# Performance work log

Measured on AMD Instinct MI355X. Metric: run time of the kernel, lower is better.

Reference implementation:

```python
import jax, jax.numpy as jnp
import numpy as np

E = 1_600_000   # edges
D = 64          # edge feature dim
H = 128         # mlp hidden
N = 100_000     # nodes


def setup_inputs() -> dict:
    key = jax.random.key(0)
    k1, k2, k3, k4 = jax.random.split(key, 4)
    edge_index = jax.random.randint(k1, (2, E), 0, N, dtype=jnp.int64)
    edge_attr = jax.random.normal(k2, (E, D), dtype=jnp.float32)
    W1 = jax.random.normal(k3, (D, H), dtype=jnp.float32) / np.sqrt(D).astype(np.float32)
    b1 = jnp.zeros((H,), jnp.float32)
    W2 = jax.random.normal(k4, (H, D), dtype=jnp.float32) / np.sqrt(H).astype(np.float32)
    b2 = jnp.zeros((D,), jnp.float32)
    return {"edge_index": edge_index, "edge_attr": edge_attr, "num_nodes": N,
            "W1": W1, "b1": b1, "W2": W2, "b2": b2}


def reference(edge_index, edge_attr, num_nodes, W1, b1, W2, b2):
    # past_nodes, future_nodes = edge_index
    past, future = edge_index[0], edge_index[1]
    # vstack((edge_attr, edge_attr)) scattered by cat((future, past)) with reduce='sum'
    src = jnp.concatenate([edge_attr, edge_attr], axis=0)          # [2E, D]
    idx = jnp.concatenate([future, past], axis=0)                  # [2E]
    flow_total = jax.ops.segment_sum(src, idx, num_segments=num_nodes)  # [N, D]
    # node_mlp: Linear(D,H) -> ReLU -> Linear(H,D)
    h = jax.nn.relu(flow_total @ W1 + b1)
    return h @ W2 + b2
```

## Files before the change

kernel.cpp:

```cpp
#include <hip/hip_runtime.h>
#include <cstdint>
#include <cstddef>

#define D_FEAT 64
#define H_HID 128

#define NBK_SHIFT 9
#define NBK_MASK 511
#define MAXBKT 256
#define TILE 8192
#define CAP 18432


__global__ __launch_bounds__(1024) void bktcount_kernel(
    const int* __restrict__ idx, int* __restrict__ bktCnt, int twoE) {
  __shared__ int cnt[MAXBKT];
  if (threadIdx.x < MAXBKT) cnt[threadIdx.x] = 0;
  __syncthreads();
  int base = blockIdx.x * TILE;
#pragma unroll
  for (int k = 0; k < TILE / 1024; ++k) {
    int t = base + k * 1024 + threadIdx.x;
    if (t < twoE) atomicAdd(&cnt[idx[t] >> NBK_SHIFT], 1);
  }
  __syncthreads();
  if (threadIdx.x < MAXBKT) {
    int c = cnt[threadIdx.x];
    if (c) atomicAdd(&bktCnt[threadIdx.x], c);
  }
}

__global__ __launch_bounds__(256) void bktscan_kernel(
    const int* __restrict__ bktCnt, int* __restrict__ bktOff,
    int* __restrict__ bktCur, int nbkt) {
  __shared__ int s[256];
  int v = (threadIdx.x < nbkt) ? bktCnt[threadIdx.x] : 0;
  s[threadIdx.x] = v;
  __syncthreads();
  for (int d = 1; d < 256; d <<= 1) {
    int t = (threadIdx.x >= d) ? s[threadIdx.x - d] : 0;
    __syncthreads();
    s[threadIdx.x] += t;
    __syncthreads();
  }
  if (threadIdx.x < nbkt) {
    int e = s[threadIdx.x] - v;
    bktOff[threadIdx.x] = e;
    bktCur[threadIdx.x] = e;
  }
}

__global__ __launch_bounds__(1024) void bktscatter_kernel(
    const int* __restrict__ idx, int* __restrict__ bktCur,
    unsigned int* __restrict__ gbkt, int E, int twoE) {
  __shared__ int cnt[MAXBKT];
  __shared__ int lofs[MAXBKT];
  __shared__ int delta[MAXBKT];
  __shared__ unsigned int sval[TILE];
  __shared__ unsigned short sbid[TILE];

  if (threadIdx.x < MAXBKT) cnt[threadIdx.x] = 0;
  __syncthreads();

  int base = blockIdx.x * TILE;
  int myb[8], myr[8];
  unsigned int myv[8];
  int m = 0;
#pragma unroll
  for (int k = 0; k < 8; ++k) {
    int t = base + k * 1024 + threadIdx.x;
    if (t < twoE) {
      int node = idx[t];
      int b = node >> NBK_SHIFT;
      int e = (t < E) ? t : t - E;
      myb[m] = b;
      myv[m] = ((unsigned int)(node & NBK_MASK) << 21) | (unsigned int)e;
      myr[m] = atomicAdd(&cnt[b], 1);
      ++m;
    }
  }
  __syncthreads();

  {
    int v = (threadIdx.x < MAXBKT) ? cnt[threadIdx.x] : 0;
    if (threadIdx.x < MAXBKT) lofs[threadIdx.x] = v;
    __syncthreads();
    for (int d = 1; d < MAXBKT; d <<= 1) {
      int t = (threadIdx.x >= d && threadIdx.x < MAXBKT) ? lofs[threadIdx.x - d] : 0;
      __syncthreads();
      if (threadIdx.x < MAXBKT) lofs[threadIdx.x] += t;
      __syncthreads();
    }
    if (threadIdx.x < MAXBKT) lofs[threadIdx.x] -= v;
  }
  __syncthreads();

  if (threadIdx.x < MAXBKT) {
    int c = cnt[threadIdx.x];
    int rb = c ? atomicAdd(&bktCur[threadIdx.x], c) : 0;
    delta[threadIdx.x] = rb - lofs[threadIdx.x];
  }
  __syncthreads();

  for (int k = 0; k < m; ++k) {
    int slot = lofs[myb[k]] + myr[k];
    sval[slot] = myv[k];
    sbid[slot] = (unsigned short)myb[k];
  }
  __syncthreads();

  int tot = min(TILE, twoE - base);
  for (int s = threadIdx.x; s < tot; s += 1024) {
    gbkt[delta[sbid[s]] + s] = sval[s];
  }
}

__global__ __launch_bounds__(1024) void bktsort_kernel(
    const int* __restrict__ bktCnt, const int* __restrict__ bktOff,
    unsigned int* __restrict__ gbkt,
    int* __restrict__ deg, int* __restrict__ off_end, int N) {
  __shared__ int hist[512];
  __shared__ int cur[512];
  __shared__ unsigned int sorted[CAP];

  int b = blockIdx.x;
  int base = bktOff[b];
  int sz = bktCnt[b];
  if (sz > CAP) sz = CAP;

  if (threadIdx.x < 512) hist[threadIdx.x] = 0;
  __syncthreads();

  for (int s = threadIdx.x; s < sz; s += 1024)
    atomicAdd(&hist[gbkt[base + s] >> 21], 1);
  __syncthreads();

  {
    int v = (threadIdx.x < 512) ? hist[threadIdx.x] : 0;
    if (threadIdx.x < 512) cur[threadIdx.x] = v;
    __syncthreads();
    for (int d = 1; d < 512; d <<= 1) {
      int t = (threadIdx.x >= d && threadIdx.x < 512) ? cur[threadIdx.x - d] : 0;
      __syncthreads();
      if (threadIdx.x < 512) cur[threadIdx.x] += t;
      __syncthreads();
    }
    if (threadIdx.x < 512) cur[threadIdx.x] -= v;
  }
  __syncthreads();

  for (int s = threadIdx.x; s < sz; s += 1024) {
    unsigned int v = gbkt[base + s];
    int p = atomicAdd(&cur[v >> 21], 1);
    if (p < CAP) sorted[p] = v & 0x1FFFFFu;
  }
  __syncthreads();

  for (int s = threadIdx.x; s < sz; s += 1024)
    gbkt[base + s] = sorted[s];

  if (threadIdx.x < 512) {
    int n = (b << NBK_SHIFT) + threadIdx.x;
    if (n < N) {
      deg[n] = hist[threadIdx.x];
      off_end[n] = base + cur[threadIdx.x];
    }
  }
}

__global__ __launch_bounds__(256) void gather_kernel(
    const int* __restrict__ deg, const int* __restrict__ off_end,
    const int* __restrict__ elist, const float* __restrict__ attr,
    float* __restrict__ flow, int N) {
  int wave = threadIdx.x >> 6;
  int lane = threadIdx.x & 63;
  int n = blockIdx.x * 4 + wave;
  if (n >= N) return;

  int end = off_end[n];
  int start = end - deg[n];
  int g = lane >> 4;
  int l = lane & 15;

  float a0 = 0.f, a1 = 0.f, a2 = 0.f, a3 = 0.f;
  int p = start + g;
  for (; p + 4 < end; p += 8) {
    int e0 = elist[p];
    int e1 = elist[p + 4];
    float4 v0 = reinterpret_cast<const float4*>(attr)[(size_t)e0 * 16 + l];
    float4 v1 = reinterpret_cast<const float4*>(attr)[(size_t)e1 * 16 + l];
    a0 += v0.x + v1.x; a1 += v0.y + v1.y;
    a2 += v0.z + v1.z; a3 += v0.w + v1.w;
  }
  if (p < end) {
    int e0 = elist[p];
    float4 v0 = reinterpret_cast<const float4*>(attr)[(size_t)e0 * 16 + l];
    a0 += v0.x; a1 += v0.y; a2 += v0.z; a3 += v0.w;
  }
  a0 += __shfl_xor(a0, 16); a0 += __shfl_xor(a0, 32);
  a1 += __shfl_xor(a1, 16); a1 += __shfl_xor(a1, 32);
  a2 += __shfl_xor(a2, 16); a2 += __shfl_xor(a2, 32);
  a3 += __shfl_xor(a3, 16); a3 += __shfl_xor(a3, 32);

  if (g == 0) {
    reinterpret_cast<float4*>(flow)[(size_t)n * 16 + l] =
        make_float4(a0, a1, a2, a3);
  }
}

__global__ __launch_bounds__(256, 2) void mlp4_kernel(
    const float* __restrict__ W1, const float* __restrict__ b1,
    const float* __restrict__ W2, const float* __restrict__ b2,
    float* __restrict__ out, int N) {
  __shared__ __align__(16) float sW1[64 * 160];
  __shared__ __align__(16) float sW2[4 * 2056];
  __shared__ __align__(16) float sB1[H_HID];
  __shared__ __align__(16) float sB2[D_FEAT];

  for (int t = threadIdx.x; t < 64 * 128; t += 256) {
    int i = t >> 7, k = t & 127;
    sW1[i * 160 + (k >> 5) * 40 + (k & 31)] = W1[t];
  }
  for (int t = threadIdx.x; t < 128 * 64; t += 256) {
    int k = t >> 6, j = t & 63;
    sW2[(k >> 5) * 2056 + (k & 31) * 64 + j] = W2[t];
  }
  if (threadIdx.x < H_HID) sB1[threadIdx.x] = b1[threadIdx.x];
  if (threadIdx.x < D_FEAT) sB2[threadIdx.x] = b2[threadIdx.x];
  __syncthreads();

  int n = blockIdx.x * 64 + (threadIdx.x >> 2);
  int q = threadIdx.x & 3;
  if (n >= N) return;

  const float* xrow = out + (size_t)n * D_FEAT;

  float h[32];
  {
    const float4* b1q = reinterpret_cast<const float4*>(sB1 + (q << 5));
#pragma unroll
    for (int v = 0; v < 8; ++v) {
      float4 b = b1q[v];
      h[4 * v + 0] = b.x; h[4 * v + 1] = b.y;
      h[4 * v + 2] = b.z; h[4 * v + 3] = b.w;
    }
  }
  const float* w1q = sW1 + q * 40;
  for (int ii = 0; ii < 16; ++ii) {
    float4 x4 = reinterpret_cast<const float4*>(xrow)[ii];
    const float* wr = w1q + (ii * 4) * 160;
#pragma unroll
    for (int u = 0; u < 4; ++u) {
      float xi = (u == 0) ? x4.x : (u == 1) ? x4.y : (u == 2) ? x4.z : x4.w;
      const float* w = wr + u * 160;
#pragma unroll
      for (int r = 0; r < 32; r += 4) {
        float4 w4 = *reinterpret_cast<const float4*>(w + r);
        h[r + 0] = fmaf(xi, w4.x, h[r + 0]);
        h[r + 1] = fmaf(xi, w4.y, h[r + 1]);
        h[r + 2] = fmaf(xi, w4.z, h[r + 2]);
        h[r + 3] = fmaf(xi, w4.w, h[r + 3]);
      }
    }
  }
#pragma unroll
  for (int r = 0; r < 32; ++r) h[r] = fmaxf(h[r], 0.f);

  float acc[64];
#pragma unroll
  for (int r = 0; r < 64; ++r) acc[r] = 0.f;

  const float* w2q = sW2 + q * 2056;
  int rot = (q & 1) << 4;
  int hi  = (q >> 1) << 5;

#pragma unroll
  for (int kl = 0; kl < 32; ++kl) {
    float hk = h[kl];
    const float* wr = w2q + kl * 64;
#pragma unroll
    for (int g = 0; g < 16; ++g) {
      int j = (hi ^ ((g >> 3) << 5)) | ((rot + ((g << 2) & 31)) & 31);
      float4 w4 = *reinterpret_cast<const float4*>(wr + j);
      acc[4 * g + 0] = fmaf(hk, w4.x, acc[4 * g + 0]);
      acc[4 * g + 1] = fmaf(hk, w4.y, acc[4 * g + 1]);
      acc[4 * g + 2] = fmaf(hk, w4.z, acc[4 * g + 2]);
      acc[4 * g + 3] = fmaf(hk, w4.w, acc[4 * g + 3]);
    }
  }

#pragma unroll
  for (int r = 0; r < 32; ++r) acc[r] += __shfl_xor(acc[32 + r], 2);
#pragma unroll
  for (int r = 0; r < 16; ++r) acc[r] += __shfl_xor(acc[16 + r], 1);

  float* orow = out + (size_t)n * D_FEAT + (q << 4);
  const float4* b2q = reinterpret_cast<const float4*>(sB2 + (q << 4));
#pragma unroll
  for (int v = 0; v < 4; ++v) {
    float4 b = b2q[v];
    reinterpret_cast<float4*>(orow)[v] =
        make_float4(acc[4 * v + 0] + b.x, acc[4 * v + 1] + b.y,
                    acc[4 * v + 2] + b.z, acc[4 * v + 3] + b.w);
  }
}

extern "C" void kernel_launch(void* const* d_in, const int* in_sizes, int n_in,
                              void* d_out, int out_size, void* d_ws, size_t ws_size,
                              hipStream_t stream) {
  const int*   edge_index = (const int*)d_in[0];
  const float* edge_attr  = (const float*)d_in[1];
  const float* W1         = (const float*)d_in[3];
  const float* b1         = (const float*)d_in[4];
  const float* W2         = (const float*)d_in[5];
  const float* b2         = (const float*)d_in[6];
  float* out = (float*)d_out;

  const int E = in_sizes[1] / D_FEAT;
  const int N = out_size / D_FEAT;
  const int twoE = 2 * E;
  const int nbkt = (N + NBK_MASK) >> NBK_SHIFT;
  const int ntile = (twoE + TILE - 1) / TILE;

  int* bktCnt = (int*)d_ws;
  int* bktOff = bktCnt + 256;
  int* bktCur = bktOff + 256;
  int* deg    = bktCur + 256;
  int* off_end = deg + N;
  unsigned int* gbkt = (unsigned int*)(off_end + N);

  hipMemsetAsync(bktCnt, 0, 256 * sizeof(int), stream);
  bktcount_kernel<<<ntile, 1024, 0, stream>>>(edge_index, bktCnt, twoE);
  bktscan_kernel<<<1, 256, 0, stream>>>(bktCnt, bktOff, bktCur, nbkt);
  bktscatter_kernel<<<ntile, 1024, 0, stream>>>(edge_index, bktCur, gbkt, E, twoE);
  bktsort_kernel<<<nbkt, 1024, 0, stream>>>(bktCnt, bktOff, gbkt, deg, off_end, N);

  gather_kernel<<<(N + 3) / 4, 256, 0, stream>>>(deg, off_end,
                                                 (const int*)gbkt, edge_attr,
                                                 out, N);
  mlp4_kernel<<<(N + 63) / 64, 256, 0, stream>>>(W1, b1, W2, b2, out, N);
}
```

Measured before the change: 726.0 us.

## Fuse bucket aggregation with node MLP using shared-memory atomic accumulation

Drops the per-bucket counting sort, the per-node gather kernel and the separate MLP kernel. One block per 256-node bucket now accumulates edge features into a shared-memory flow tile with LDS float atomics, then runs the two-layer MLP directly from shared memory. Bucket width is halved (512 buckets) so the flow tile fits in LDS. This removes the in-bucket sort pass, the flow round trip through global memory and two launches. In exchange it adds LDS atomic contention, only 391 blocks for the whole fused stage, heavy LDS use that allows one block per CU, and a summation order that is no longer deterministic.

New measurement: 1.864 ms. 157% more time.

```diff
diff --git a/kernel.cpp b/kernel.cpp
--- a/kernel.cpp
+++ b/kernel.cpp
@@ -5,11 +5,11 @@
 #define D_FEAT 64
 #define H_HID 128
 
-#define NBK_SHIFT 9
-#define NBK_MASK 511
-#define MAXBKT 256
+#define NBK_SHIFT 8
+#define NBK_MASK 255
+#define MAXBKT 512
 #define TILE 8192
-#define CAP 18432
+#define FSTRIDE 68
 
 
 __global__ __launch_bounds__(1024) void bktcount_kernel(
@@ -30,14 +30,14 @@
   }
 }
 
-__global__ __launch_bounds__(256) void bktscan_kernel(
+__global__ __launch_bounds__(512) void bktscan_kernel(
     const int* __restrict__ bktCnt, int* __restrict__ bktOff,
     int* __restrict__ bktCur, int nbkt) {
-  __shared__ int s[256];
+  __shared__ int s[MAXBKT];
   int v = (threadIdx.x < nbkt) ? bktCnt[threadIdx.x] : 0;
   s[threadIdx.x] = v;
   __syncthreads();
-  for (int d = 1; d < 256; d <<= 1) {
+  for (int d = 1; d < MAXBKT; d <<= 1) {
     int t = (threadIdx.x >= d) ? s[threadIdx.x - d] : 0;
     __syncthreads();
     s[threadIdx.x] += t;
@@ -115,134 +115,71 @@
   }
 }
 
-__global__ __launch_bounds__(1024) void bktsort_kernel(
+__global__ __launch_bounds__(1024, 1) void agg_mlp_kernel(
     const int* __restrict__ bktCnt, const int* __restrict__ bktOff,
-    unsigned int* __restrict__ gbkt,
-    int* __restrict__ deg, int* __restrict__ off_end, int N) {
-  __shared__ int hist[512];
-  __shared__ int cur[512];
-  __shared__ unsigned int sorted[CAP];
-
-  int b = blockIdx.x;
-  int base = bktOff[b];
-  int sz = bktCnt[b];
-  if (sz > CAP) sz = CAP;
-
-  if (threadIdx.x < 512) hist[threadIdx.x] = 0;
-  __syncthreads();
-
-  for (int s = threadIdx.x; s < sz; s += 1024)
-    atomicAdd(&hist[gbkt[base + s] >> 21], 1);
-  __syncthreads();
-
-  {
-    int v = (threadIdx.x < 512) ? hist[threadIdx.x] : 0;
-    if (threadIdx.x < 512) cur[threadIdx.x] = v;
-    __syncthreads();
-    for (int d = 1; d < 512; d <<= 1) {
-      int t = (threadIdx.x >= d && threadIdx.x < 512) ? cur[threadIdx.x - d] : 0;
-      __syncthreads();
-      if (threadIdx.x < 512) cur[threadIdx.x] += t;
-      __syncthreads();
-    }
-    if (threadIdx.x < 512) cur[threadIdx.x] -= v;
-  }
-  __syncthreads();
-
-  for (int s = threadIdx.x; s < sz; s += 1024) {
-    unsigned int v = gbkt[base + s];
-    int p = atomicAdd(&cur[v >> 21], 1);
-    if (p < CAP) sorted[p] = v & 0x1FFFFFu;
-  }
-  __syncthreads();
-
-  for (int s = threadIdx.x; s < sz; s += 1024)
-    gbkt[base + s] = sorted[s];
-
-  if (threadIdx.x < 512) {
-    int n = (b << NBK_SHIFT) + threadIdx.x;
-    if (n < N) {
-      deg[n] = hist[threadIdx.x];
-      off_end[n] = base + cur[threadIdx.x];
-    }
-  }
-}
-
-__global__ __launch_bounds__(256) void gather_kernel(
-    const int* __restrict__ deg, const int* __restrict__ off_end,
-    const int* __restrict__ elist, const float* __restrict__ attr,
-    float* __restrict__ flow, int N) {
-  int wave = threadIdx.x >> 6;
-  int lane = threadIdx.x & 63;
-  int n = blockIdx.x * 4 + wave;
-  if (n >= N) return;
-
-  int end = off_end[n];
-  int start = end - deg[n];
-  int g = lane >> 4;
-  int l = lane & 15;
-
-  float a0 = 0.f, a1 = 0.f, a2 = 0.f, a3 = 0.f;
-  int p = start + g;
-  for (; p + 4 < end; p += 8) {
-    int e0 = elist[p];
-    int e1 = elist[p + 4];
-    float4 v0 = reinterpret_cast<const float4*>(attr)[(size_t)e0 * 16 + l];
-    float4 v1 = reinterpret_cast<const float4*>(attr)[(size_t)e1 * 16 + l];
-    a0 += v0.x + v1.x; a1 += v0.y + v1.y;
-    a2 += v0.z + v1.z; a3 += v0.w + v1.w;
-  }
-  if (p < end) {
-    int e0 = elist[p];
-    float4 v0 = reinterpret_cast<const float4*>(attr)[(size_t)e0 * 16 + l];
-    a0 += v0.x; a1 += v0.y; a2 += v0.z; a3 += v0.w;
-  }
-  a0 += __shfl_xor(a0, 16); a0 += __shfl_xor(a0, 32);
-  a1 += __shfl_xor(a1, 16); a1 += __shfl_xor(a1, 32);
-  a2 += __shfl_xor(a2, 16); a2 += __shfl_xor(a2, 32);
-  a3 += __shfl_xor(a3, 16); a3 += __shfl_xor(a3, 32);
-
-  if (g == 0) {
-    reinterpret_cast<float4*>(flow)[(size_t)n * 16 + l] =
-        make_float4(a0, a1, a2, a3);
-  }
-}
-
-__global__ __launch_bounds__(256, 2) void mlp4_kernel(
+    const unsigned int* __restrict__ gbkt, const float* __restrict__ attr,
     const float* __restrict__ W1, const float* __restrict__ b1,
     const float* __restrict__ W2, const float* __restrict__ b2,
     float* __restrict__ out, int N) {
+  __shared__ __align__(16) float sFlow[256 * FSTRIDE];
   __shared__ __align__(16) float sW1[64 * 160];
   __shared__ __align__(16) float sW2[4 * 2056];
   __shared__ __align__(16) float sB1[H_HID];
   __shared__ __align__(16) float sB2[D_FEAT];
 
-  for (int t = threadIdx.x; t < 64 * 128; t += 256) {
+  for (int t = threadIdx.x; t < 64 * 128; t += 1024) {
     int i = t >> 7, k = t & 127;
     sW1[i * 160 + (k >> 5) * 40 + (k & 31)] = W1[t];
   }
-  for (int t = threadIdx.x; t < 128 * 64; t += 256) {
+  for (int t = threadIdx.x; t < 128 * 64; t += 1024) {
     int k = t >> 6, j = t & 63;
     sW2[(k >> 5) * 2056 + (k & 31) * 64 + j] = W2[t];
   }
   if (threadIdx.x < H_HID) sB1[threadIdx.x] = b1[threadIdx.x];
   if (threadIdx.x < D_FEAT) sB2[threadIdx.x] = b2[threadIdx.x];
-  __syncthreads();
-
-  int n = blockIdx.x * 64 + (threadIdx.x >> 2);
+  {
+    float4 z = make_float4(0.f, 0.f, 0.f, 0.f);
+    float4* f4 = reinterpret_cast<float4*>(sFlow);
+    for (int v = threadIdx.x; v < (256 * FSTRIDE) / 4; v += 1024) f4[v] = z;
+  }
+  __syncthreads();
+
+  int b = blockIdx.x;
+  int base = bktOff[b];
+  int sz = bktCnt[b];
+
+  {
+    int grp = threadIdx.x >> 4;
+    int l = threadIdx.x & 15;
+    for (int s = grp; s < sz; s += 64) {
+      unsigned int v = gbkt[base + s];
+      int ln = v >> 21;
+      int e = (int)(v & 0x1FFFFFu);
+      float4 a = reinterpret_cast<const float4*>(attr)[(size_t)e * 16 + l];
+      float* dst = &sFlow[ln * FSTRIDE + l * 4];
+      atomicAdd(dst + 0, a.x);
+      atomicAdd(dst + 1, a.y);
+      atomicAdd(dst + 2, a.z);
+      atomicAdd(dst + 3, a.w);
+    }
+  }
+  __syncthreads();
+
+  int ln = threadIdx.x >> 2;
   int q = threadIdx.x & 3;
+  int n = (b << NBK_SHIFT) + ln;
   if (n >= N) return;
 
-  const float* xrow = out + (size_t)n * D_FEAT;
+  const float* xrow = &sFlow[ln * FSTRIDE];
 
   float h[32];
   {
     const float4* b1q = reinterpret_cast<const float4*>(sB1 + (q << 5));
 #pragma unroll
     for (int v = 0; v < 8; ++v) {
-      float4 b = b1q[v];
-      h[4 * v + 0] = b.x; h[4 * v + 1] = b.y;
-      h[4 * v + 2] = b.z; h[4 * v + 3] = b.w;
+      float4 bb = b1q[v];
+      h[4 * v + 0] = bb.x; h[4 * v + 1] = bb.y;
+      h[4 * v + 2] = bb.z; h[4 * v + 3] = bb.w;
     }
   }
   const float* w1q = sW1 + q * 40;
@@ -298,10 +235,10 @@
   const float4* b2q = reinterpret_cast<const float4*>(sB2 + (q << 4));
 #pragma unroll
   for (int v = 0; v < 4; ++v) {
-    float4 b = b2q[v];
+    float4 bb = b2q[v];
     reinterpret_cast<float4*>(orow)[v] =
-        make_float4(acc[4 * v + 0] + b.x, acc[4 * v + 1] + b.y,
-                    acc[4 * v + 2] + b.z, acc[4 * v + 3] + b.w);
+        make_float4(acc[4 * v + 0] + bb.x, acc[4 * v + 1] + bb.y,
+                    acc[4 * v + 2] + bb.z, acc[4 * v + 3] + bb.w);
   }
 }
 
@@ -323,20 +260,14 @@
   const int ntile = (twoE + TILE - 1) / TILE;
 
   int* bktCnt = (int*)d_ws;
-  int* bktOff = bktCnt + 256;
-  int* bktCur = bktOff + 256;
-  int* deg    = bktCur + 256;
-  int* off_end = deg + N;
-  unsigned int* gbkt = (unsigned int*)(off_end + N);
-
-  hipMemsetAsync(bktCnt, 0, 256 * sizeof(int), stream);
+  int* bktOff = bktCnt + MAXBKT;
+  int* bktCur = bktOff + MAXBKT;
+  unsigned int* gbkt = (unsigned int*)(bktCur + MAXBKT);
+
+  hipMemsetAsync(bktCnt, 0, MAXBKT * sizeof(int), stream);
   bktcount_kernel<<<ntile, 1024, 0, stream>>>(edge_index, bktCnt, twoE);
-  bktscan_kernel<<<1, 256, 0, stream>>>(bktCnt, bktOff, bktCur, nbkt);
+  bktscan_kernel<<<1, MAXBKT, 0, stream>>>(bktCnt, bktOff, bktCur, nbkt);
   bktscatter_kernel<<<ntile, 1024, 0, stream>>>(edge_index, bktCur, gbkt, E, twoE);
-  bktsort_kernel<<<nbkt, 1024, 0, stream>>>(bktCnt, bktOff, gbkt, deg, off_end, N);
-
-  gather_kernel<<<(N + 3) / 4, 256, 0, stream>>>(deg, off_end,
-                                                 (const int*)gbkt, edge_attr,
-                                                 out, N);
-  mlp4_kernel<<<(N + 63) / 64, 256, 0, stream>>>(W1, b1, W2, b2, out, N);
-}
+  agg_mlp_kernel<<<nbkt, 1024, 0, stream>>>(bktCnt, bktOff, gbkt, edge_attr,
+                                            W1, b1, W2, b2, out, N);
+}
```
